# Kernel optimization log

Measured on AMD Instinct MI355X. Metric: run time of the kernel, lower is better.

The kernel has to match this reference:

```python
import jax, jax.numpy as jnp
import numpy as np

RADIUS = 2  # half window; original kernel truncates the spatial Gaussian at ~2.5*sigma


def setup_inputs() -> dict:
    key = jax.random.key(0)
    input_img = jax.random.normal(key, (2, 1, 128, 128, 128), dtype=jnp.float32)
    return {
        "input_img": input_img,
        "sigma_x": jnp.float32(1.0),
        "sigma_y": jnp.float32(1.0),
        "sigma_z": jnp.float32(1.0),
        "color_sigma": jnp.float32(0.5),
    }


def reference(input_img, sigma_x, sigma_y, sigma_z, color_sigma):
    # 3D bilateral filter: out(i) = sum_k w_spatial(k) * w_range(x_i, x_k) * x_k / sum_k w
    R = RADIUS
    pad = [(0, 0), (0, 0), (R, R), (R, R), (R, R)]
    xp = jnp.pad(input_img, pad)                       # zero-padded volume
    mp = jnp.pad(jnp.ones_like(input_img), pad)        # validity mask (out-of-bounds taps excluded)

    offs = np.array([(dx, dy, dz)
                     for dx in range(-R, R + 1)
                     for dy in range(-R, R + 1)
                     for dz in range(-R, R + 1)], dtype=np.int32)  # (K,3), K=125
    d2 = jnp.asarray(offs.astype(np.float32) ** 2)     # squared offsets (K,3)
    w_sp = jnp.exp(-(d2[:, 0] / (2.0 * sigma_x ** 2)
                     + d2[:, 1] / (2.0 * sigma_y ** 2)
                     + d2[:, 2] / (2.0 * sigma_z ** 2)))  # (K,)
    starts = jnp.asarray(offs + R)                     # slice starts into the padded volume

    inv_2cs2 = 1.0 / (2.0 * color_sigma ** 2)
    shape = input_img.shape

    def body(carry, inp):
        num, den = carry
        start, ws = inp
        s = jnp.concatenate([jnp.zeros(2, jnp.int32), start])
        xk = jax.lax.dynamic_slice(xp, s, shape)       # shifted neighbor volume
        mk = jax.lax.dynamic_slice(mp, s, shape)
        w = ws * mk * jnp.exp(-(input_img - xk) ** 2 * inv_2cs2)
        return (num + w * xk, den + w), None

    zero = jnp.zeros_like(input_img)
    (num, den), _ = jax.lax.scan(body, (zero, zero), (starts, w_sp))
    return num / den
```

## Files before the change

### kernel.cpp

```cpp
#include <hip/hip_runtime.h>
#include <hip/hip_bf16.h>


#define RADIUS 2
#define N 128
#define TX 16
#define TY 8
#define TZ 8
#define PITCH (TX + 2 * RADIUS)
#define LYD (TY + 2 * RADIUS)
#define LZD (TZ + 2 * RADIUS)
#define LDS_SIZE (PITCH * LYD * LZD)

#define LOG2E 1.4426950408889634f
#define BIG 1.0e18f
#define EXP2_SCALE 8388608.0f
#define EXP2_BIAS 1065353216.0f

__global__ __launch_bounds__(256, 4) void bilateral3d_kernel(
    const float* __restrict__ in, const float* __restrict__ p_sx,
    const float* __restrict__ p_sy, const float* __restrict__ p_sz,
    const float* __restrict__ p_cs, float* __restrict__ out) {
  __shared__ float s[LDS_SIZE];

  const int tid = threadIdx.x;
  const int x0 = blockIdx.x * TX;
  const int y0 = blockIdx.y * TY;
  const int zb = blockIdx.z;
  const int z0 = (zb & 15) * TZ;
  const int b = zb >> 4;

  const float sxv = p_sx[0], syv = p_sy[0], szv = p_sz[0], csv = p_cs[0];
  const float AX2 = EXP2_SCALE * LOG2E / (2.0f * sxv * sxv);
  const float AY2 = EXP2_SCALE * LOG2E / (2.0f * syv * syv);
  const float AZ2 = EXP2_SCALE * LOG2E / (2.0f * szv * szv);
  const float AX2_4 = 4.0f * AX2;
  const float sR = __builtin_sqrtf(EXP2_SCALE * LOG2E / (2.0f * csv * csv));

  const float* vol = in + (size_t)b * (N * N * N);

  for (int i = tid; i < LDS_SIZE; i += 256) {
    int lx = i % PITCH;
    int t = i / PITCH;
    int ly = t % LYD;
    int lz = t / LYD;
    int gx = x0 + lx - RADIUS;
    int gy = y0 + ly - RADIUS;
    int gz = z0 + lz - RADIUS;
    float v = BIG;
    if ((unsigned)gx < N && (unsigned)gy < N && (unsigned)gz < N)
      v = vol[((size_t)gz * N + gy) * N + gx];
    s[i] = v * sR;
  }
  __syncthreads();

  const int ty = tid & 7;
  const int tx = (tid >> 3) & 3;
  const int tz = tid >> 5;

  const int xw = 4 * tx;

  const int cbase = ((tz + RADIUS) * LYD + (ty + RADIUS)) * PITCH + xw;
  const float4 CA = *(const float4*)&s[cbase];
  const float4 CB = *(const float4*)&s[cbase + 4];
  const float xc0 = CA.z, xc1 = CA.w, xc2 = CB.x, xc3 = CB.y;

  float n0 = 0, n1 = 0, n2 = 0, n3 = 0;
  float e0 = 0, e1 = 0, e2 = 0, e3 = 0;

#define TAP(XC, FV, CC, NN, DD)                          \
  {                                                      \
    float _t = (XC) - (FV);                              \
    float _f = fmaf(_t, -_t, (CC));                      \
    unsigned _q;                                         \
    asm("v_cvt_u32_f32 %0, %1" : "=v"(_q) : "v"(_f));    \
    float _w = __uint_as_float(_q);                      \
    DD += _w;                                            \
    NN = fmaf(_w, (FV), NN);                             \
  }

#pragma unroll 1
  for (int dz = -RADIUS; dz <= RADIUS; ++dz) {
    const float pz2 = AZ2 * (float)(dz * dz);
    const int zrow = (tz + RADIUS + dz) * LYD;
#pragma unroll
    for (int dy = -RADIUS; dy <= RADIUS; ++dy) {
      const float cc0 = EXP2_BIAS - (pz2 + AY2 * (float)(dy * dy));
      const float cm1 = cc0 - AX2;
      const float cm4 = cc0 - AX2_4;
      const int rb = (zrow + (ty + RADIUS + dy)) * PITCH + xw;
      const float4 A = *(const float4*)&s[rb];
      const float4 B = *(const float4*)&s[rb + 4];
      const float f0 = A.x, f1 = A.y, f2 = A.z, f3 = A.w;
      const float f4 = B.x, f5 = B.y, f6 = B.z, f7 = B.w;

      TAP(xc0, f0, cm4, n0, e0)
      TAP(xc1, f1, cm4, n1, e1)
      TAP(xc2, f2, cm4, n2, e2)
      TAP(xc3, f3, cm4, n3, e3)
      TAP(xc0, f1, cm1, n0, e0)
      TAP(xc1, f2, cm1, n1, e1)
      TAP(xc2, f3, cm1, n2, e2)
      TAP(xc3, f4, cm1, n3, e3)
      TAP(xc0, f2, cc0, n0, e0)
      TAP(xc1, f3, cc0, n1, e1)
      TAP(xc2, f4, cc0, n2, e2)
      TAP(xc3, f5, cc0, n3, e3)
      TAP(xc0, f3, cm1, n0, e0)
      TAP(xc1, f4, cm1, n1, e1)
      TAP(xc2, f5, cm1, n2, e2)
      TAP(xc3, f6, cm1, n3, e3)
      TAP(xc0, f4, cm4, n0, e0)
      TAP(xc1, f5, cm4, n1, e1)
      TAP(xc2, f6, cm4, n2, e2)
      TAP(xc3, f7, cm4, n3, e3)
    }
  }

  float4 r;
  r.x = n0 / (e0 * sR);
  r.y = n1 / (e1 * sR);
  r.z = n2 / (e2 * sR);
  r.w = n3 / (e3 * sR);

  const int gz = z0 + tz, gy = y0 + ty;
  *(float4*)&out[(((size_t)b * N + gz) * N + gy) * N + (x0 + xw)] = r;
}

extern "C" void kernel_launch(void* const* d_in, const int* in_sizes, int n_in,
                              void* d_out, int out_size, void* d_ws, size_t ws_size,
                              hipStream_t stream) {
  const float* in = (const float*)d_in[0];
  const float* sx = (const float*)d_in[1];
  const float* sy = (const float*)d_in[2];
  const float* sz = (const float*)d_in[3];
  const float* cs = (const float*)d_in[4];
  float* out = (float*)d_out;

  dim3 grid(N / TX, N / TY, (N / TZ) * 2);
  bilateral3d_kernel<<<grid, 256, 0, stream>>>(in, sx, sy, sz, cs, out);
}
```

Baseline: 137.0 us.

## Compute two y-rows per thread to reuse LDS row loads across outputs

Each thread now produces two adjacent y outputs (4 x-values each), and the block tile grows to 16 in y. Each loaded LDS row is shared between the two output rows, which cuts LDS reads per output by about 40% and amortizes the halo load over a larger tile. The cost is higher register pressure from the doubled accumulators and centre values, half as many blocks in the grid, and possible spills under launch_bounds(256,4).

```diff
diff --git a/kernel.cpp b/kernel.cpp
--- a/kernel.cpp
+++ b/kernel.cpp
@@ -5,7 +5,7 @@
 #define RADIUS 2
 #define N 128
 #define TX 16
-#define TY 8
+#define TY 16
 #define TZ 8
 #define PITCH (TX + 2 * RADIUS)
 #define LYD (TY + 2 * RADIUS)
@@ -35,6 +35,7 @@
   const float AY2 = EXP2_SCALE * LOG2E / (2.0f * syv * syv);
   const float AZ2 = EXP2_SCALE * LOG2E / (2.0f * szv * szv);
   const float AX2_4 = 4.0f * AX2;
+  const float py1 = AY2, py4 = 4.0f * AY2;
   const float sR = __builtin_sqrtf(EXP2_SCALE * LOG2E / (2.0f * csv * csv));
 
   const float* vol = in + (size_t)b * (N * N * N);
@@ -59,14 +60,20 @@
   const int tz = tid >> 5;
 
   const int xw = 4 * tx;
+  const int yc = 2 * ty + RADIUS;
 
-  const int cbase = ((tz + RADIUS) * LYD + (ty + RADIUS)) * PITCH + xw;
-  const float4 CA = *(const float4*)&s[cbase];
-  const float4 CB = *(const float4*)&s[cbase + 4];
-  const float xc0 = CA.z, xc1 = CA.w, xc2 = CB.x, xc3 = CB.y;
+  const int cbA = ((tz + RADIUS) * LYD + yc) * PITCH + xw;
+  const float4 CAa = *(const float4*)&s[cbA];
+  const float4 CBa = *(const float4*)&s[cbA + 4];
+  const float xca0 = CAa.z, xca1 = CAa.w, xca2 = CBa.x, xca3 = CBa.y;
+  const float4 CAb = *(const float4*)&s[cbA + PITCH];
+  const float4 CBb = *(const float4*)&s[cbA + PITCH + 4];
+  const float xcb0 = CAb.z, xcb1 = CAb.w, xcb2 = CBb.x, xcb3 = CBb.y;
 
-  float n0 = 0, n1 = 0, n2 = 0, n3 = 0;
-  float e0 = 0, e1 = 0, e2 = 0, e3 = 0;
+  float na0 = 0, na1 = 0, na2 = 0, na3 = 0;
+  float ea0 = 0, ea1 = 0, ea2 = 0, ea3 = 0;
+  float nb0 = 0, nb1 = 0, nb2 = 0, nb3 = 0;
+  float eb0 = 0, eb1 = 0, eb2 = 0, eb3 = 0;
 
 #define TAP(XC, FV, CC, NN, DD)                          \
   {                                                      \
@@ -79,52 +86,68 @@
     NN = fmaf(_w, (FV), NN);                             \
   }
 
+#define DOROW(S, PY)                                     \
+  {                                                      \
+    const float cc0 = bz - (PY);                         \
+    const float cm1 = cc0 - AX2;                         \
+    const float cm4 = cc0 - AX2_4;                       \
+    TAP(xc##S##0, f0, cm4, n##S##0, e##S##0)             \
+    TAP(xc##S##1, f1, cm4, n##S##1, e##S##1)             \
+    TAP(xc##S##2, f2, cm4, n##S##2, e##S##2)             \
+    TAP(xc##S##3, f3, cm4, n##S##3, e##S##3)             \
+    TAP(xc##S##0, f1, cm1, n##S##0, e##S##0)             \
+    TAP(xc##S##1, f2, cm1, n##S##1, e##S##1)             \
+    TAP(xc##S##2, f3, cm1, n##S##2, e##S##2)             \
+    TAP(xc##S##3, f4, cm1, n##S##3, e##S##3)             \
+    TAP(xc##S##0, f2, cc0, n##S##0, e##S##0)             \
+    TAP(xc##S##1, f3, cc0, n##S##1, e##S##1)             \
+    TAP(xc##S##2, f4, cc0, n##S##2, e##S##2)             \
+    TAP(xc##S##3, f5, cc0, n##S##3, e##S##3)             \
+    TAP(xc##S##0, f3, cm1, n##S##0, e##S##0)             \
+    TAP(xc##S##1, f4, cm1, n##S##1, e##S##1)             \
+    TAP(xc##S##2, f5, cm1, n##S##2, e##S##2)             \
+    TAP(xc##S##3, f6, cm1, n##S##3, e##S##3)             \
+    TAP(xc##S##0, f4, cm4, n##S##0, e##S##0)             \
+    TAP(xc##S##1, f5, cm4, n##S##1, e##S##1)             \
+    TAP(xc##S##2, f6, cm4, n##S##2, e##S##2)             \
+    TAP(xc##S##3, f7, cm4, n##S##3, e##S##3)             \
+  }
+
+#define LOADROW(J)                                                \
+    const int rb = (zrow + yc + (J)) * PITCH + xw;                \
+    const float4 A = *(const float4*)&s[rb];                      \
+    const float4 B = *(const float4*)&s[rb + 4];                  \
+    const float f0 = A.x, f1 = A.y, f2 = A.z, f3 = A.w;           \
+    const float f4 = B.x, f5 = B.y, f6 = B.z, f7 = B.w;
+
 #pragma unroll 1
   for (int dz = -RADIUS; dz <= RADIUS; ++dz) {
-    const float pz2 = AZ2 * (float)(dz * dz);
+    const float bz = EXP2_BIAS - AZ2 * (float)(dz * dz);
     const int zrow = (tz + RADIUS + dz) * LYD;
-#pragma unroll
-    for (int dy = -RADIUS; dy <= RADIUS; ++dy) {
-      const float cc0 = EXP2_BIAS - (pz2 + AY2 * (float)(dy * dy));
-      const float cm1 = cc0 - AX2;
-      const float cm4 = cc0 - AX2_4;
-      const int rb = (zrow + (ty + RADIUS + dy)) * PITCH + xw;
-      const float4 A = *(const float4*)&s[rb];
-      const float4 B = *(const float4*)&s[rb + 4];
-      const float f0 = A.x, f1 = A.y, f2 = A.z, f3 = A.w;
-      const float f4 = B.x, f5 = B.y, f6 = B.z, f7 = B.w;
 
-      TAP(xc0, f0, cm4, n0, e0)
-      TAP(xc1, f1, cm4, n1, e1)
-      TAP(xc2, f2, cm4, n2, e2)
-      TAP(xc3, f3, cm4, n3, e3)
-      TAP(xc0, f1, cm1, n0, e0)
-      TAP(xc1, f2, cm1, n1, e1)
-      TAP(xc2, f3, cm1, n2, e2)
-      TAP(xc3, f4, cm1, n3, e3)
-      TAP(xc0, f2, cc0, n0, e0)
-      TAP(xc1, f3, cc0, n1, e1)
-      TAP(xc2, f4, cc0, n2, e2)
-      TAP(xc3, f5, cc0, n3, e3)
-      TAP(xc0, f3, cm1, n0, e0)
-      TAP(xc1, f4, cm1, n1, e1)
-      TAP(xc2, f5, cm1, n2, e2)
-      TAP(xc3, f6, cm1, n3, e3)
-      TAP(xc0, f4, cm4, n0, e0)
-      TAP(xc1, f5, cm4, n1, e1)
-      TAP(xc2, f6, cm4, n2, e2)
-      TAP(xc3, f7, cm4, n3, e3)
-    }
+    { LOADROW(-2) DOROW(a, py4) }
+    { LOADROW(-1) DOROW(a, py1) DOROW(b, py4) }
+    { LOADROW(0)  DOROW(a, 0.0f) DOROW(b, py1) }
+    { LOADROW(1)  DOROW(a, py1) DOROW(b, 0.0f) }
+    { LOADROW(2)  DOROW(a, py4) DOROW(b, py1) }
+    { LOADROW(3)  DOROW(b, py4) }
   }
 
-  float4 r;
-  r.x = n0 / (e0 * sR);
-  r.y = n1 / (e1 * sR);
-  r.z = n2 / (e2 * sR);
-  r.w = n3 / (e3 * sR);
+  const int gz = z0 + tz;
+  const int gya = y0 + 2 * ty;
+  float4 ra, rbv;
+  ra.x = na0 / (ea0 * sR);
+  ra.y = na1 / (ea1 * sR);
+  ra.z = na2 / (ea2 * sR);
+  ra.w = na3 / (ea3 * sR);
+  rbv.x = nb0 / (eb0 * sR);
+  rbv.y = nb1 / (eb1 * sR);
+  rbv.z = nb2 / (eb2 * sR);
+  rbv.w = nb3 / (eb3 * sR);
 
-  const int gz = z0 + tz, gy = y0 + ty;
-  *(float4*)&out[(((size_t)b * N + gz) * N + gy) * N + (x0 + xw)] = r;
+  float* op = &out[(((size_t)b * N + gz) * N + gya) * N + (x0 + xw)];
+  *(float4*)op = ra;
+  *(float4*)(op + N) = rbv;
 }
 
 extern "C" void kernel_launch(void* const* d_in, const int* in_sizes, int n_in,
```

Result: slower. 142.8 us (+4.2%).
